# Optimization experiments

Measured on AMD Instinct MI355X. Metric: run time of the kernel, lower is better.

Reference implementation:

```python
import jax, jax.numpy as jnp
import numpy as np
import math

B, N, K, C = 2, 8192, 16, 64
PE_DIM, HID = 32, 16
SIGMA, EPS = 1.0, 1e-06


def setup_inputs() -> dict:
    key = jax.random.key(0)
    ks = jax.random.split(key, 8)
    p = jax.random.normal(ks[0], (B, N, 3), jnp.float32)
    f = jax.random.normal(ks[1], (B, C, N), jnp.float32)
    pe = jax.random.normal(ks[2], (B, C, N, K), jnp.float32)
    knn_idx = jax.random.randint(ks[3], (B, N, K), 0, N, jnp.int32)
    # LocalAggregation convs1: 1x1 conv [C -> C] (+ReLU)
    W1 = jax.random.normal(ks[4], (C, C), jnp.float32) * (1.0 / math.sqrt(C))
    b1 = jnp.zeros((C,), jnp.float32)
    # GaussianKDEOffsetGenerator params: pe_mlp Linear(3->32), ffn Linear(32->16)->Linear(16->3)
    Wpe = jax.random.normal(ks[5], (PE_DIM, 3), jnp.float32) * (1.0 / math.sqrt(3))
    bpe = jnp.zeros((PE_DIM,), jnp.float32)
    Wh1 = jax.random.normal(ks[6], (HID, PE_DIM), jnp.float32) * (1.0 / math.sqrt(PE_DIM))
    bh1 = jnp.zeros((HID,), jnp.float32)
    Wh2 = jax.random.normal(ks[7], (3, HID), jnp.float32) * (1.0 / math.sqrt(HID))
    bh2 = jnp.zeros((3,), jnp.float32)
    return {"p": p, "f": f, "pe": pe, "W1": W1, "b1": b1, "Wpe": Wpe,
            "bpe": bpe, "Wh1": Wh1, "bh1": bh1, "Wh2": Wh2, "bh2": bh2,
            "knn_idx": knn_idx}


def reference(p, f, pe, W1, b1, Wpe, bpe, Wh1, bh1, Wh2, bh2, knn_idx):
    gather = jax.vmap(lambda a, i: a[i])  # per-batch neighbor gather
    # --- LocalAggregation: convs1 (1x1 conv + relu), group_by_idx, pe+fj, max-pool over K ---
    h = jax.nn.relu(jnp.einsum('oc,bcn->bon', W1, f) + b1[None, :, None])  # [B,C,N]
    ht = jnp.transpose(h, (0, 2, 1))                                       # [B,N,C]
    fj = gather(ht, knn_idx)                                               # [B,N,K,C]
    fout = jnp.max(pe + jnp.transpose(fj, (0, 3, 1, 2)), axis=-1)          # [B,C,N]
    # --- GaussianKDEOffsetGenerator on grouped neighbor coords [B*N, K, 3] ---
    coords = gather(p, knn_idx).reshape(B * N, K, 3)
    rel = coords[:, :, None, :] - coords[:, None, :, :]                    # [BN,K,K,3]
    pek = jax.nn.relu(jnp.einsum('nijc,dc->nijd', rel, Wpe) + bpe).mean(axis=2)  # [BN,K,PE]
    dist2 = jnp.sum(rel * rel, axis=-1)                                    # [BN,K,K]
    coef = 1.0 / math.sqrt(2.0 * math.pi * SIGMA ** 2 + EPS)
    kde = (coef * jnp.exp(-dist2 / (2.0 * SIGMA ** 2 + EPS))).sum(axis=2, keepdims=True)
    kde = kde / (jnp.max(kde, axis=1, keepdims=True) + EPS)                # [BN,K,1]
    fused = pek * kde
    delta = jax.nn.relu(fused @ Wh1.T + bh1) @ Wh2.T + bh2                 # [BN,K,3]
    return (fout, delta)
```

## Files before the change

kernel.cpp:

```cpp
#include <hip/hip_runtime.h>

#define B_ 2
#define N_ 8192
#define K_ 16
#define C_ 64
#define PE_ 32
#define HID_ 16

typedef float f4 __attribute__((ext_vector_type(4)));

__device__ __forceinline__ f4 splat4(float x) { f4 r = {x, x, x, x}; return r; }
__device__ __forceinline__ f4 relu4(f4 v) {
  f4 r;
  r[0] = fmaxf(v[0], 0.f); r[1] = fmaxf(v[1], 0.f);
  r[2] = fmaxf(v[2], 0.f); r[3] = fmaxf(v[3], 0.f);
  return r;
}
__device__ __forceinline__ float dot4(float4 w, f4 v) {
  return fmaf(w.x, v[0], fmaf(w.y, v[1], fmaf(w.z, v[2], w.w * v[3])));
}

struct PK4 { f4 k0, k1, k2, k3; };

__device__ __forceinline__ PK4 channel(const float4* __restrict__ sq,
                                       int d, const float* __restrict__ Wpe,
                                       const float* __restrict__ bpe) {
  const float wx = Wpe[d * 3 + 0], wy = Wpe[d * 3 + 1], wz = Wpe[d * 3 + 2];
  const float wb = bpe[d];
  const float4 A0 = sq[0], B0 = sq[1], C0 = sq[2];
  const float4 A1 = sq[3], B1 = sq[4], C1 = sq[5];
  const float4 A2 = sq[6], B2 = sq[7], C2 = sq[8];
  const float4 A3 = sq[9], B3 = sq[10], C3 = sq[11];
  const float p0  = fmaf(wx, A0.x, fmaf(wy, A0.y, wz * A0.z));
  const float p1  = fmaf(wx, A0.w, fmaf(wy, B0.x, wz * B0.y));
  const float p2  = fmaf(wx, B0.z, fmaf(wy, B0.w, wz * C0.x));
  const float p3  = fmaf(wx, C0.y, fmaf(wy, C0.z, wz * C0.w));
  const float p4  = fmaf(wx, A1.x, fmaf(wy, A1.y, wz * A1.z));
  const float p5  = fmaf(wx, A1.w, fmaf(wy, B1.x, wz * B1.y));
  const float p6  = fmaf(wx, B1.z, fmaf(wy, B1.w, wz * C1.x));
  const float p7  = fmaf(wx, C1.y, fmaf(wy, C1.z, wz * C1.w));
  const float p8  = fmaf(wx, A2.x, fmaf(wy, A2.y, wz * A2.z));
  const float p9  = fmaf(wx, A2.w, fmaf(wy, B2.x, wz * B2.y));
  const float p10 = fmaf(wx, B2.z, fmaf(wy, B2.w, wz * C2.x));
  const float p11 = fmaf(wx, C2.y, fmaf(wy, C2.z, wz * C2.w));
  const float p12 = fmaf(wx, A3.x, fmaf(wy, A3.y, wz * A3.z));
  const float p13 = fmaf(wx, A3.w, fmaf(wy, B3.x, wz * B3.y));
  const float p14 = fmaf(wx, B3.z, fmaf(wy, B3.w, wz * C3.x));
  const float p15 = fmaf(wx, C3.y, fmaf(wy, C3.z, wz * C3.w));
  const f4 a0 = {p0 + wb, p1 + wb, p2 + wb, p3 + wb};
  const f4 a1 = {p4 + wb, p5 + wb, p6 + wb, p7 + wb};
  const f4 a2 = {p8 + wb, p9 + wb, p10 + wb, p11 + wb};
  const f4 a3 = {p12 + wb, p13 + wb, p14 + wb, p15 + wb};
  f4 k0 = splat4(0.f), k1 = splat4(0.f), k2 = splat4(0.f), k3 = splat4(0.f);
#define KSTEP(PJ)                                  \
  {                                                \
    const f4 sp = splat4(PJ);                      \
    k0 += relu4(a0 - sp); k1 += relu4(a1 - sp);    \
    k2 += relu4(a2 - sp); k3 += relu4(a3 - sp);    \
  }
  KSTEP(p0) KSTEP(p1) KSTEP(p2) KSTEP(p3) KSTEP(p4) KSTEP(p5) KSTEP(p6)
  KSTEP(p7) KSTEP(p8) KSTEP(p9) KSTEP(p10) KSTEP(p11) KSTEP(p12) KSTEP(p13)
  KSTEP(p14) KSTEP(p15)
#undef KSTEP
  PK4 r; r.k0 = k0; r.k1 = k1; r.k2 = k2; r.k3 = k3;
  return r;
}

__global__ __launch_bounds__(256) void k1v3(
    const float* __restrict__ f, const float* __restrict__ W1,
    const float* __restrict__ b1, float* __restrict__ ht) {
  __shared__ float sf[C_ * 20];
  const int t = threadIdx.x;
  const int g0 = blockIdx.x * 16;
  const int b = g0 >> 13;
  const int n0 = g0 & (N_ - 1);
  {
    const int c = t >> 2, off = (t & 3) * 4;
    const f4 v = *reinterpret_cast<const f4*>(f + (size_t)(b * C_ + c) * N_ + n0 + off);
    *reinterpret_cast<f4*>(&sf[c * 20 + off]) = v;
  }
  __syncthreads();
  const int lane = t & 63;
  const int w = t >> 6;
  const f4* wp = reinterpret_cast<const f4*>(W1 + lane * C_);
  const f4 w0 = wp[0], w1 = wp[1], w2 = wp[2], w3 = wp[3];
  const f4 w4 = wp[4], w5 = wp[5], w6 = wp[6], w7 = wp[7];
  const f4 w8 = wp[8], w9 = wp[9], w10 = wp[10], w11 = wp[11];
  const f4 w12 = wp[12], w13 = wp[13], w14 = wp[14], w15 = wp[15];
  f4 a = splat4(0.f);
#define CSTEP(Q, E)                                                         \
  {                                                                         \
    const f4 fv = *reinterpret_cast<const f4*>(&sf[(Q * 4 + E) * 20 + w * 4]); \
    a += splat4(w##Q[E]) * fv;                                              \
  }
#define CQ(Q) CSTEP(Q, 0) CSTEP(Q, 1) CSTEP(Q, 2) CSTEP(Q, 3)
  CQ(0) CQ(1) CQ(2) CQ(3) CQ(4) CQ(5) CQ(6) CQ(7)
  CQ(8) CQ(9) CQ(10) CQ(11) CQ(12) CQ(13) CQ(14) CQ(15)
#undef CQ
#undef CSTEP
  const float bias = b1[lane];
  #pragma unroll
  for (int pt = 0; pt < 4; ++pt)
    ht[(size_t)(b * N_ + n0 + w * 4 + pt) * C_ + lane] = fmaxf(a[pt] + bias, 0.f);
}

#define SFJ_STRIDE 65
#define SOUT_OFF 16640
#define NP2 1024
__global__ __launch_bounds__(256) void k23_split(
    const float* __restrict__ p, const float* __restrict__ pe,
    const float* __restrict__ ht, const int* __restrict__ knn,
    const float* __restrict__ Wpe, const float* __restrict__ bpe,
    const float* __restrict__ Wh1, const float* __restrict__ bh1,
    const float* __restrict__ Wh2, const float* __restrict__ bh2,
    float* __restrict__ fout, float* __restrict__ delta) {
  __shared__ __align__(16) char smem[21760];
  const int t = threadIdx.x;

  if (blockIdx.x < NP2) {
    float* sfj = (float*)smem;
    float* sout = (float*)(smem + SOUT_OFF);
    const int base = blockIdx.x * 16;
    const int b = base >> 13;
    const int n0b = base & (N_ - 1);
    const int lane = t & 63;
    const int w = t >> 6;
    const int csub = lane >> 4, sl = lane & 15;
    const int j = sl & 3, nn = sl >> 2;
    #pragma unroll 1
    for (int si = 0; si < 4; ++si) {
      const int n0 = n0b + si * 4;
      #pragma unroll
      for (int n = 0; n < 4; ++n) {
        const int* kn = knn + (size_t)(b * N_ + n0 + n) * K_ + w * 4;
        #pragma unroll
        for (int kk = 0; kk < 4; ++kk) {
          const int id = kn[kk];
          const float hv = ht[(size_t)(b * N_ + id) * C_ + lane];
          sfj[lane * SFJ_STRIDE + (n * 4 + w) * 4 + kk] = hv;
        }
      }
      __syncthreads();
      #pragma unroll
      for (int it2 = 0; it2 < 4; ++it2) {
        const int c = it2 * 16 + w * 4 + csub;
        const f4 pv = *(reinterpret_cast<const f4*>(
            pe + ((size_t)(b * C_ + c) * N_ + n0) * K_) + sl);
        const f4 fj = *reinterpret_cast<const f4*>(&sfj[c * SFJ_STRIDE + sl * 4]);
        float v = fmaxf(fmaxf(pv[0] + fj[0], pv[1] + fj[1]),
                        fmaxf(pv[2] + fj[2], pv[3] + fj[3]));
        v = fmaxf(v, __shfl_xor(v, 1));
        v = fmaxf(v, __shfl_xor(v, 2));
        if (j == 0) sout[c * 20 + si * 4 + nn] = v;
      }
      __syncthreads();
    }
    const int c = t >> 2, q = t & 3;
    const float4 r = *reinterpret_cast<const float4*>(&sout[c * 20 + q * 4]);
    *reinterpret_cast<float4*>(fout + (size_t)(b * C_ + c) * N_ + n0b + q * 4) = r;
    return;
  }

  {
    float* spk = (float*)smem;
    float* sc = (float*)(smem + 16384);
    const int base = (blockIdx.x - NP2) * 8;
    const int b = base >> 13;
    const int g = t >> 5;
    const int l = t & 31;

    if (l < 16) {
      const int gid = base + g;
      const int idx = knn[(size_t)gid * K_ + l];
      const float* pp = p + (size_t)(b * N_ + idx) * 3;
      sc[g * 48 + l * 3 + 0] = pp[0];
      sc[g * 48 + l * 3 + 1] = pp[1];
      sc[g * 48 + l * 3 + 2] = pp[2];
    }
    __syncthreads();

    {
      const int d = l;
      const float4* sq = reinterpret_cast<const float4*>(&sc[g * 48]);
      const PK4 ck = channel(sq, d, Wpe, bpe);
      const int qw = d >> 2, pos = d & 3;
      float* gbase = spk + g * 512;
#define PKW(II, KV) \
      gbase[(II) * 32 + (((qw ^ ((II) & 7)) << 2) | pos)] = ck.KV[(II) & 3];
      PKW(0, k0) PKW(1, k0) PKW(2, k0) PKW(3, k0)
      PKW(4, k1) PKW(5, k1) PKW(6, k1) PKW(7, k1)
      PKW(8, k2) PKW(9, k2) PKW(10, k2) PKW(11, k2)
      PKW(12, k3) PKW(13, k3) PKW(14, k3) PKW(15, k3)
#undef PKW
    }
    __syncthreads();

    {
      const int i = t & 15, half = (t >> 4) & 1;
      const int gid = base + g;
      const float ci0 = sc[g * 48 + i * 3 + 0];
      const float ci1 = sc[g * 48 + i * 3 + 1];
      const float ci2 = sc[g * 48 + i * 3 + 2];
      const float4* sq = reinterpret_cast<const float4*>(&sc[g * 48]);
      const float INV2S = 0.49999975f;
      const float COEF = 0.39894225f;
      float kacc = 0.f;
      #pragma unroll
      for (int jj = 0; jj < 2; ++jj) {
        const int j4 = half * 2 + jj;
        const float4 a = sq[j4 * 3 + 0], b4 = sq[j4 * 3 + 1], c4 = sq[j4 * 3 + 2];
        float dx, dy, dz;
        dx = ci0 - a.x;  dy = ci1 - a.y;  dz = ci2 - a.z;
        kacc += __expf(-(dx * dx + dy * dy + dz * dz) * INV2S);
        dx = ci0 - a.w;  dy = ci1 - b4.x; dz = ci2 - b4.y;
        kacc += __expf(-(dx * dx + dy * dy + dz * dz) * INV2S);
        dx = ci0 - b4.z; dy = ci1 - b4.w; dz = ci2 - c4.x;
        kacc += __expf(-(dx * dx + dy * dy + dz * dz) * INV2S);
        dx = ci0 - c4.y; dy = ci1 - c4.z; dz = ci2 - c4.w;
        kacc += __expf(-(dx * dx + dy * dy + dz * dz) * INV2S);
      }
      kacc += __shfl_xor(kacc, 16);
      const float kde = COEF * kacc;
      float m = kde;
      m = fmaxf(m, __shfl_xor(m, 1));
      m = fmaxf(m, __shfl_xor(m, 2));
      m = fmaxf(m, __shfl_xor(m, 4));
      m = fmaxf(m, __shfl_xor(m, 8));
      const float s = (kde / (m + 1e-6f)) * (1.f / 16.f);

      const float* rbase = spk + g * 512 + i * 32;
      const int ix = i & 7;
      const f4 v0 = *reinterpret_cast<const f4*>(&rbase[(0 ^ ix) << 2]);
      const f4 v1 = *reinterpret_cast<const f4*>(&rbase[(1 ^ ix) << 2]);
      const f4 v2 = *reinterpret_cast<const f4*>(&rbase[(2 ^ ix) << 2]);
      const f4 v3 = *reinterpret_cast<const f4*>(&rbase[(3 ^ ix) << 2]);
      const f4 v4 = *reinterpret_cast<const f4*>(&rbase[(4 ^ ix) << 2]);
      const f4 v5 = *reinterpret_cast<const f4*>(&rbase[(5 ^ ix) << 2]);
      const f4 v6 = *reinterpret_cast<const f4*>(&rbase[(6 ^ ix) << 2]);
      const f4 v7 = *reinterpret_cast<const f4*>(&rbase[(7 ^ ix) << 2]);

      float o0 = 0.f, o1 = 0.f, o2 = 0.f;
      #pragma unroll
      for (int hh = 0; hh < 8; ++hh) {
        const int h = half * 8 + hh;
        const float4* Wr = reinterpret_cast<const float4*>(Wh1 + h * PE_);
        const float u = dot4(Wr[0], v0) + dot4(Wr[1], v1) + dot4(Wr[2], v2) +
                        dot4(Wr[3], v3) + dot4(Wr[4], v4) + dot4(Wr[5], v5) +
                        dot4(Wr[6], v6) + dot4(Wr[7], v7);
        const float a = fmaxf(fmaf(s, u, bh1[h]), 0.f);
        o0 = fmaf(Wh2[0 * HID_ + h], a, o0);
        o1 = fmaf(Wh2[1 * HID_ + h], a, o1);
        o2 = fmaf(Wh2[2 * HID_ + h], a, o2);
      }
      o0 += __shfl_xor(o0, 16);
      o1 += __shfl_xor(o1, 16);
      o2 += __shfl_xor(o2, 16);
      if (half == 0) {
        float* dp = delta + ((size_t)gid * K_ + i) * 3;
        dp[0] = o0 + bh2[0];
        dp[1] = o1 + bh2[1];
        dp[2] = o2 + bh2[2];
      }
    }
  }
}

extern "C" void kernel_launch(void* const* d_in, const int* in_sizes, int n_in,
                              void* d_out, int out_size, void* d_ws, size_t ws_size,
                              hipStream_t stream) {
  const float* p   = (const float*)d_in[0];
  const float* f   = (const float*)d_in[1];
  const float* pe  = (const float*)d_in[2];
  const float* W1  = (const float*)d_in[3];
  const float* b1  = (const float*)d_in[4];
  const float* Wpe = (const float*)d_in[5];
  const float* bpe = (const float*)d_in[6];
  const float* Wh1 = (const float*)d_in[7];
  const float* bh1 = (const float*)d_in[8];
  const float* Wh2 = (const float*)d_in[9];
  const float* bh2 = (const float*)d_in[10];
  const int* knn   = (const int*)d_in[11];
  float* fout  = (float*)d_out;
  float* delta = (float*)d_out + (size_t)B_ * C_ * N_;
  float* ht = (float*)d_ws;

  k1v3<<<(B_ * N_) / 16, 256, 0, stream>>>(f, W1, b1, ht);
  k23_split<<<NP2 + (B_ * N_) / 8, 256, 0, stream>>>(
      p, pe, ht, knn, Wpe, bpe, Wh1, bh1, Wh2, bh2, fout, delta);
}
```

Baseline: 55.55 us.

## Compute fout max per thread directly, dropping shared-memory gather staging

Result: slower. 65.38 us (+17.7%).

```diff
diff --git a/kernel.cpp b/kernel.cpp
--- a/kernel.cpp
+++ b/kernel.cpp
@@ -104,8 +104,6 @@
     ht[(size_t)(b * N_ + n0 + w * 4 + pt) * C_ + lane] = fmaxf(a[pt] + bias, 0.f);
 }
 
-#define SFJ_STRIDE 65
-#define SOUT_OFF 16640
 #define NP2 1024
 __global__ __launch_bounds__(256) void k23_split(
     const float* __restrict__ p, const float* __restrict__ pe,
@@ -114,49 +112,37 @@
     const float* __restrict__ Wh1, const float* __restrict__ bh1,
     const float* __restrict__ Wh2, const float* __restrict__ bh2,
     float* __restrict__ fout, float* __restrict__ delta) {
-  __shared__ __align__(16) char smem[21760];
+  __shared__ __align__(16) char smem[17920];
   const int t = threadIdx.x;
 
   if (blockIdx.x < NP2) {
-    float* sfj = (float*)smem;
-    float* sout = (float*)(smem + SOUT_OFF);
+    float* sout = (float*)smem;
     const int base = blockIdx.x * 16;
     const int b = base >> 13;
     const int n0b = base & (N_ - 1);
     const int lane = t & 63;
     const int w = t >> 6;
-    const int csub = lane >> 4, sl = lane & 15;
-    const int j = sl & 3, nn = sl >> 2;
-    #pragma unroll 1
-    for (int si = 0; si < 4; ++si) {
-      const int n0 = n0b + si * 4;
+    #pragma unroll
+    for (int pt = 0; pt < 4; ++pt) {
+      const int n = n0b + w * 4 + pt;
+      const int* kn = knn + (size_t)(b * N_ + n) * K_;
+      const f4* per = reinterpret_cast<const f4*>(
+          pe + ((size_t)(b * C_ + lane) * N_ + n) * K_);
+      const f4 q0 = per[0], q1 = per[1], q2 = per[2], q3 = per[3];
+      float mx = -3.402823466e+38f;
       #pragma unroll
-      for (int n = 0; n < 4; ++n) {
-        const int* kn = knn + (size_t)(b * N_ + n0 + n) * K_ + w * 4;
-        #pragma unroll
-        for (int kk = 0; kk < 4; ++kk) {
-          const int id = kn[kk];
-          const float hv = ht[(size_t)(b * N_ + id) * C_ + lane];
-          sfj[lane * SFJ_STRIDE + (n * 4 + w) * 4 + kk] = hv;
-        }
-      }
-      __syncthreads();
-      #pragma unroll
-      for (int it2 = 0; it2 < 4; ++it2) {
-        const int c = it2 * 16 + w * 4 + csub;
-        const f4 pv = *(reinterpret_cast<const f4*>(
-            pe + ((size_t)(b * C_ + c) * N_ + n0) * K_) + sl);
-        const f4 fj = *reinterpret_cast<const f4*>(&sfj[c * SFJ_STRIDE + sl * 4]);
-        float v = fmaxf(fmaxf(pv[0] + fj[0], pv[1] + fj[1]),
-                        fmaxf(pv[2] + fj[2], pv[3] + fj[3]));
-        v = fmaxf(v, __shfl_xor(v, 1));
-        v = fmaxf(v, __shfl_xor(v, 2));
-        if (j == 0) sout[c * 20 + si * 4 + nn] = v;
-      }
-      __syncthreads();
-    }
+      for (int k = 0; k < K_; ++k) {
+        const float hv = ht[(size_t)(b * N_ + kn[k]) * C_ + lane];
+        const float pv = (k < 4) ? q0[k & 3] : (k < 8) ? q1[k & 3]
+                        : (k < 12) ? q2[k & 3] : q3[k & 3];
+        mx = fmaxf(mx, pv + hv);
+      }
+      sout[lane * 18 + w * 4 + pt] = mx;
+    }
+    __syncthreads();
     const int c = t >> 2, q = t & 3;
-    const float4 r = *reinterpret_cast<const float4*>(&sout[c * 20 + q * 4]);
+    const float4 r = make_float4(sout[c * 18 + q * 4 + 0], sout[c * 18 + q * 4 + 1],
+                                 sout[c * 18 + q * 4 + 2], sout[c * 18 + q * 4 + 3]);
     *reinterpret_cast<float4*>(fout + (size_t)(b * C_ + c) * N_ + n0b + q * 4) = r;
     return;
   }
```
